# Optimization experiments

Measured on AMD Instinct MI355X. Metric: run time of the kernel, lower is better.

## Reference

```python
import jax, jax.numpy as jnp
from jax import lax
import numpy as np

C = 64          # channels
E = 8           # num_experts
K = 2           # active_experts
P = 8           # patch_size
EPS = 1e-5


def setup_inputs() -> dict:
    key = jax.random.key(0)
    ks = jax.random.split(key, 12)
    s = 0.05
    inp = {
        "x": jax.random.normal(ks[0], (2, C, 8, 128, 128), dtype=jnp.float32),
        # router Linear(C, E)
        "router_w": jax.random.normal(ks[1], (E, C), dtype=jnp.float32) * s,
        "router_b": jnp.zeros((E,), dtype=jnp.float32),
        # per-expert GatedConvBlock params, stacked over E
        "dw_w": jax.random.normal(ks[2], (E, C, 1, 1, 7, 7), dtype=jnp.float32) * s,   # depthwise (1,7,7)
        "dw_b": jnp.zeros((E, C), dtype=jnp.float32),
        "ln_w": jnp.ones((E, P, P), dtype=jnp.float32),
        "ln_b": jnp.zeros((E, P, P), dtype=jnp.float32),
        "pw_in_w": jax.random.normal(ks[3], (E, 2 * C, C), dtype=jnp.float32) * s,
        "pw_in_b": jnp.zeros((E, 2 * C), dtype=jnp.float32),
        "pw_out_w": jax.random.normal(ks[4], (E, C, C), dtype=jnp.float32) * s,
        "pw_out_b": jnp.zeros((E, C), dtype=jnp.float32),
    }
    return inp


def _gated_conv_block(x, dw_w, dw_b, ln_w, ln_b, pw_in_w, pw_in_b, pw_out_w, pw_out_b):
    # x: [N, C, L, P, P]
    res = x
    h = lax.conv_general_dilated(
        x, dw_w, window_strides=(1, 1, 1), padding="SAME",
        feature_group_count=x.shape[1],
        dimension_numbers=("NCDHW", "OIDHW", "NCDHW"),
    ) + dw_b[None, :, None, None, None]
    # LayerNorm over last two (spatial) dims with affine of shape [P, P]
    mu = jnp.mean(h, axis=(-2, -1), keepdims=True)
    var = jnp.var(h, axis=(-2, -1), keepdims=True)
    h = (h - mu) * lax.rsqrt(var + EPS) * ln_w + ln_b
    # pointwise conv in (1x1x1): C -> 2C
    h2 = jnp.einsum("oc,ncdhw->nodhw", pw_in_w, h) + pw_in_b[None, :, None, None, None]
    a, g = jnp.split(h2, 2, axis=1)
    h = jax.nn.silu(a) * g
    # pointwise conv out: C -> C
    h = jnp.einsum("oc,ncdhw->nodhw", pw_out_w, h) + pw_out_b[None, :, None, None, None]
    return res + h


def reference(x, router_w, router_b, dw_w, dw_b, ln_w, ln_b,
              pw_in_w, pw_in_b, pw_out_w, pw_out_b):
    B, Cc, L, H, W = x.shape
    nH, nW = H // P, W // P  # H, W chosen divisible by P (no padding path)
    N = B * nH * nW
    # patchify: [B,C,L,H,W] -> [N, C, L, P, P]
    xp = x.reshape(B, Cc, L, nH, P, nW, P).transpose(0, 3, 5, 1, 2, 4, 6)
    xp = xp.reshape(N, Cc, L, P, P)
    # router: mean over (L, P, P)
    router_in = jnp.mean(xp, axis=(2, 3, 4))                      # [N, C]
    logits = router_in @ router_w.T + router_b                    # [N, E]
    topv, topi = lax.top_k(logits, K)                             # [N, K]
    topw = jax.nn.softmax(topv, axis=1)                           # [N, K]
    # scatter top-k weights to dense [N, E] (zeros for unselected experts)
    wfull = jnp.zeros((N, E), dtype=x.dtype)
    wfull = wfull.at[jnp.arange(N)[:, None], topi].add(topw)
    out = jnp.zeros_like(xp)
    for e in range(E):  # fixed small expert count; each expert has distinct params
        ye = _gated_conv_block(xp, dw_w[e], dw_b[e], ln_w[e], ln_b[e],
                               pw_in_w[e], pw_in_b[e], pw_out_w[e], pw_out_b[e])
        out = out + wfull[:, e][:, None, None, None, None] * ye
    # unpatchify
    out = out.reshape(B, nH, nW, Cc, L, P, P).transpose(0, 3, 4, 1, 5, 2, 6)
    return out.reshape(B, Cc, L, H, W)
```

## Files before the change

kernel.cpp:

```cpp
#include <hip/hip_runtime.h>
#include <hip/hip_bf16.h>
#include <cstddef>
#include <cstdint>


typedef __attribute__((ext_vector_type(8))) short short8;
typedef __attribute__((ext_vector_type(4))) float f32x4;
typedef __attribute__((ext_vector_type(2))) float f32x2;

#define REPACK_NEED 68412416ull

__device__ __forceinline__ unsigned short f2bf(float f) {
  return __builtin_bit_cast(unsigned short, __float2bfloat16(f));
}
__device__ __forceinline__ float bflo(unsigned u) {
  return __builtin_bit_cast(float, u << 16);
}
__device__ __forceinline__ float bfhi(unsigned u) {
  return __builtin_bit_cast(float, u & 0xFFFF0000u);
}

__device__ __forceinline__ float wave_sum64(float v) {
#pragma unroll
  for (int m = 32; m > 0; m >>= 1) v += __shfl_xor(v, m, 64);
  return v;
}

__global__ void k_pre(const float* __restrict__ dw,
                      const float* __restrict__ pwin,
                      const float* __restrict__ pwout,
                      unsigned short* __restrict__ dwTbf,
                      unsigned short* __restrict__ wIn,
                      unsigned short* __restrict__ wOut) {
  int idx = blockIdx.x * 256 + threadIdx.x;
  if (idx < 25088) {
    int e = idx / 3136;
    int r = idx - e * 3136;
    int c = r / 49;
    int tap = r - c * 49;
    dwTbf[(e * 49 + tap) * 64 + c] = f2bf(dw[idx]);
  } else if (idx < 25088 + 65536) {
    int i = idx - 25088;
    wIn[i] = f2bf(pwin[i]);
  } else if (idx < 25088 + 65536 + 32768) {
    int i = idx - 90624;
    wOut[i] = f2bf(pwout[i]);
  }
}

__global__ __launch_bounds__(256) void k_sum(const float* __restrict__ x,
                                             float* __restrict__ partial_l) {
  __shared__ float red[256 * 17];
  int t = threadIdx.x, bid = blockIdx.x;
  int b = bid >> 8, c = (bid >> 2) & 63, lp = bid & 3;
  const float4* x4 = (const float4*)x + ((size_t)((b * 64 + c) * 8) + lp * 2) * 4096;
#pragma unroll 1
  for (int l2 = 0; l2 < 2; ++l2) {
    float acc[16];
#pragma unroll
    for (int k = 0; k < 16; ++k) acc[k] = 0.f;
#pragma unroll
    for (int k = 0; k < 16; ++k) {
      float4 v = x4[l2 * 4096 + k * 256 + t];
      acc[k] += v.x + v.y + v.z + v.w;
    }
    int pcol = (t & 31) >> 1;
    int slot = ((t & 1) << 3) | (t >> 5);
    __syncthreads();
#pragma unroll
    for (int k = 0; k < 16; ++k) red[(k * 16 + pcol) * 17 + slot] = acc[k];
    __syncthreads();
    float s = 0.f;
#pragma unroll
    for (int j = 0; j < 16; ++j) s += red[t * 17 + j];
    partial_l[((size_t)(b * 256 + t)) * 512 + (lp * 2 + l2) * 64 + c] = s;
  }
}

__global__ __launch_bounds__(256) void k_repack(const float* __restrict__ x,
                                                float* __restrict__ xr,
                                                float* __restrict__ partial_l) {
  __shared__ __align__(16) float lt[8 * 1060];
  int t = threadIdx.x, bid = blockIdx.x;
  int ct = bid & 7, hh = (bid >> 3) & 15, l = (bid >> 7) & 7, b = bid >> 10;
  int c0 = ct * 8;
  const float4* x4 = (const float4*)x;
  float4* xr4 = (float4*)xr;
  int y = t >> 5, xq = t & 31;
#pragma unroll
  for (int i = 0; i < 8; ++i) {
    size_t src = ((size_t)((b * 64 + c0 + i) * 8 + l) << 12) +
                 (size_t)(hh * 8 + y) * 32 + xq;
    float4 v = x4[src];
    *(float4*)(lt + i * 1060 + y * 132 + xq * 4) = v;
  }
  __syncthreads();
  int cc = (t >> 4) & 7, ihalf = t >> 7, pxq = t & 15;
  int py = pxq >> 1, xcol = pxq & 1;
#pragma unroll
  for (int iw = 0; iw < 8; ++iw) {
    int ww = ihalf * 8 + iw;
    float4 v = *(const float4*)(lt + cc * 1060 + py * 132 + ww * 8 + xcol * 4);
    int n = b * 256 + hh * 16 + ww;
    xr4[((size_t)(n * 8 + l) << 10) + (c0 + cc) * 16 + pxq] = v;
    float s = v.x + v.y + v.z + v.w;
#pragma unroll
    for (int m = 1; m < 16; m <<= 1) s += __shfl_xor(s, m, 64);
    if (pxq == 0) partial_l[(size_t)(n * 8 + l) * 64 + c0 + cc] = s;
  }
}

__global__ void k_router(const float* __restrict__ partial_l,
                         const float* __restrict__ rw, const float* __restrict__ rb,
                         int* __restrict__ sel_i, float* __restrict__ sel_w) {
  int n = blockIdx.x;
  int lane = threadIdx.x;
  float s = 0.f;
#pragma unroll
  for (int l = 0; l < 8; ++l)
    s += partial_l[(size_t)n * 512 + l * 64 + lane];
  float rin = s * (1.f / 512.f);
  float lg[8];
#pragma unroll
  for (int e = 0; e < 8; ++e) {
    float v = rin * rw[e * 64 + lane];
    lg[e] = wave_sum64(v) + rb[e];
  }
  int e0 = 0; float v0 = lg[0];
#pragma unroll
  for (int e = 1; e < 8; ++e) if (lg[e] > v0) { v0 = lg[e]; e0 = e; }
  int e1 = -1; float v1 = -1e30f;
#pragma unroll
  for (int e = 0; e < 8; ++e) if (e != e0 && lg[e] > v1) { v1 = lg[e]; e1 = e; }
  if (lane == 0) {
    float w1 = __expf(v1 - v0);
    float z = 1.f + w1;
    sel_i[2 * n] = e0; sel_i[2 * n + 1] = e1;
    sel_w[2 * n] = 1.f / z; sel_w[2 * n + 1] = w1 / z;
  }
}

template <bool REPACK>
__global__ __launch_bounds__(512) void k_main(
    const float* __restrict__ x, const float* __restrict__ xr,
    const unsigned short* __restrict__ dwTbf, const float* __restrict__ dwb,
    const float* __restrict__ lnw, const float* __restrict__ lnb,
    const float* __restrict__ pwin_b, const float* __restrict__ pwout_b,
    const unsigned short* __restrict__ wInBf,
    const unsigned short* __restrict__ wOutBf,
    const int* __restrict__ sel_i, const float* __restrict__ sel_w,
    float* __restrict__ out) {
  __shared__ __align__(16) char smem[49408];
  unsigned* wsdw       = (unsigned*)smem;
  unsigned short* B1   = (unsigned short*)(smem + 12544);
  unsigned short* B2   = (unsigned short*)(smem + 21760);
  unsigned short* B3   = (unsigned short*)(smem + 30976);
  f32x2* ln2           = (f32x2*)(smem + 30976);
  unsigned short* xsb  = (unsigned short*)(smem + 40192);
  float* eb            = (float*)(smem + 21760);

  const int t = threadIdx.x;
  const int lane = t & 63;
  const int wv = __builtin_amdgcn_readfirstlane(t >> 6);
  const int wi = wv >> 1;
  const int jh = wv & 1;
  const int r15 = lane & 15, r4 = lane >> 4;
  const int bidx = blockIdx.x;
  const int n = bidx >> 3, l = bidx & 7;
  const int b = n >> 8, p = n & 255;
  const int hh = p >> 4, ww = p & 15;
  const size_t obase = (size_t)b * 8388608 + (size_t)l * 16384 +
                       (size_t)hh * 1024 + (size_t)ww * 8;

  const int e0 = __builtin_amdgcn_readfirstlane(sel_i[2 * n]);
  const int e1 = __builtin_amdgcn_readfirstlane(sel_i[2 * n + 1]);
  const float we0 = sel_w[2 * n];
  const float we1 = sel_w[2 * n + 1];

#pragma unroll
  for (int it = 0; it < 2; ++it) {
    int g = it * 512 + t;
    int c = g >> 4, q = g & 15;
    float4 v;
    if constexpr (REPACK)
      v = ((const float4*)xr)[(size_t)bidx * 1024 + g];
    else
      v = *(const float4*)(x + obase + (size_t)c * 131072 + (q >> 1) * 128 + (q & 1) * 4);
    int rs = (q >> 1) ^ ((c >> 3) & 7);
    uint2 w2;
    w2.x = (unsigned)f2bf(v.x) | ((unsigned)f2bf(v.y) << 16);
    w2.y = (unsigned)f2bf(v.z) | ((unsigned)f2bf(v.w) << 16);
    *(uint2*)(xsb + c * 72 + rs * 8 + (q & 1) * 4) = w2;
  }
  {
    const unsigned short* s0 = dwTbf + (size_t)e0 * 3136;
    const unsigned short* s1 = dwTbf + (size_t)e1 * 3136;
#pragma unroll
    for (int i = 0; i < 6; ++i) {
      int idx = i * 512 + t;
      wsdw[idx] = (unsigned)s0[idx] | ((unsigned)s1[idx] << 16);
    }
    if (t < 64) wsdw[3072 + t] = (unsigned)s0[3072 + t] | ((unsigned)s1[3072 + t] << 16);
  }
  __syncthreads();

  f32x2 hva[4], hvb[4];
  {
    const float bias0 = dwb[e0 * 64 + lane];
    const float bias1 = dwb[e1 * 64 + lane];
#pragma unroll
    for (int j = 0; j < 4; ++j) {
      hva[j] = f32x2{bias0, bias0};
      hvb[j] = f32x2{bias1, bias1};
    }
  }
  {
    const unsigned short* rowbase = xsb + lane * 72;
    const int rc = (lane >> 3) & 7;
    const unsigned* wl = wsdw + lane;
    const int y0 = wv;
    const int rlo = (y0 - 3 < 0) ? 0 : y0 - 3;
    const int rhi = (y0 + 3 > 7) ? 7 : y0 + 3;
    for (int r = rlo; r <= rhi; ++r) {
      uint4 xraw = *(const uint4*)(rowbase + (r ^ rc) * 8);
      float xp[14];
      xp[0] = 0.f; xp[1] = 0.f; xp[2] = 0.f;
      xp[3] = bflo(xraw.x); xp[4] = bfhi(xraw.x);
      xp[5] = bflo(xraw.y); xp[6] = bfhi(xraw.y);
      xp[7] = bflo(xraw.z); xp[8] = bfhi(xraw.z);
      xp[9] = bflo(xraw.w); xp[10] = bfhi(xraw.w);
      xp[11] = 0.f; xp[12] = 0.f; xp[13] = 0.f;
      f32x2 pr[13];
#pragma unroll
      for (int m = 0; m < 13; ++m) pr[m] = f32x2{xp[m], xp[m + 1]};
      const unsigned* wrow = wl + (r - y0 + 3) * 448;
#pragma unroll
      for (int dx = 0; dx < 7; ++dx) {
        unsigned wp = wrow[dx * 64];
        float wt0 = bflo(wp);
        float wt1 = bfhi(wp);
        f32x2 w20 = f32x2{wt0, wt0};
        f32x2 w21 = f32x2{wt1, wt1};
        hva[0] = __builtin_elementwise_fma(pr[dx + 0], w20, hva[0]);
        hva[1] = __builtin_elementwise_fma(pr[dx + 2], w20, hva[1]);
        hva[2] = __builtin_elementwise_fma(pr[dx + 4], w20, hva[2]);
        hva[3] = __builtin_elementwise_fma(pr[dx + 6], w20, hva[3]);
        hvb[0] = __builtin_elementwise_fma(pr[dx + 0], w21, hvb[0]);
        hvb[1] = __builtin_elementwise_fma(pr[dx + 2], w21, hvb[1]);
        hvb[2] = __builtin_elementwise_fma(pr[dx + 4], w21, hvb[2]);
        hvb[3] = __builtin_elementwise_fma(pr[dx + 6], w21, hvb[3]);
      }
    }
  }
  {
    f32x2 psa = f32x2{0.f, 0.f}, pqa = f32x2{0.f, 0.f};
    f32x2 psb = f32x2{0.f, 0.f}, pqb = f32x2{0.f, 0.f};
#pragma unroll
    for (int j = 0; j < 4; ++j) {
      psa += hva[j];
      pqa = __builtin_elementwise_fma(hva[j], hva[j], pqa);
      psb += hvb[j];
      pqb = __builtin_elementwise_fma(hvb[j], hvb[j], pqb);
    }
    ln2[(0 * 8 + wv) * 64 + lane] = f32x2{psa.x + psa.y, pqa.x + pqa.y};
    ln2[(1 * 8 + wv) * 64 + lane] = f32x2{psb.x + psb.y, pqb.x + pqb.y};
  }
  __syncthreads();

  {
    float sm0 = 0.f, sq0 = 0.f, sm1 = 0.f, sq1 = 0.f;
#pragma unroll
    for (int w = 0; w < 8; ++w) {
      f32x2 va = ln2[(0 * 8 + w) * 64 + lane];
      f32x2 vb = ln2[(1 * 8 + w) * 64 + lane];
      sm0 += va.x; sq0 += va.y;
      sm1 += vb.x; sq1 += vb.y;
    }
    float mu0 = sm0 * (1.f / 64.f);
    float rstd0 = rsqrtf(sq0 * (1.f / 64.f) - mu0 * mu0 + 1e-5f);
    float mu1 = sm1 * (1.f / 64.f);
    float rstd1 = rsqrtf(sq1 * (1.f / 64.f) - mu1 * mu1 + 1e-5f);
#pragma unroll
    for (int j = 0; j < 8; ++j) {
      int s = wv * 8 + j;
      float ha = (j & 1) ? hva[j >> 1].y : hva[j >> 1].x;
      float hb = (j & 1) ? hvb[j >> 1].y : hvb[j >> 1].x;
      float nv0 = (ha - mu0) * rstd0 * lnw[e0 * 64 + s] + lnb[e0 * 64 + s];
      float nv1 = (hb - mu1) * rstd1 * lnw[e1 * 64 + s] + lnb[e1 * 64 + s];
      B1[s * 72 + lane] = f2bf(nv0);
      B2[s * 72 + lane] = f2bf(nv1);
    }
  }
  __syncthreads();

  float oacc[8];
#pragma unroll
  for (int i = 0; i < 8; ++i) oacc[i] = 0.f;

  {
    const unsigned short* wInE = wInBf + (size_t)e0 * 8192;
    short8 aA[2], aG[2];
#pragma unroll
    for (int kf = 0; kf < 2; ++kf) {
      aA[kf] = *(const short8*)(wInE + (16 * wi + r15) * 64 + kf * 32 + r4 * 8);
      aG[kf] = *(const short8*)(wInE + (64 + 16 * wi + r15) * 64 + kf * 32 + r4 * 8);
    }
    f32x4 accA[2], accG[2];
#pragma unroll
    for (int ntl = 0; ntl < 2; ++ntl)
#pragma unroll
      for (int v = 0; v < 4; ++v) {
        accA[ntl][v] = pwin_b[e0 * 128 + 16 * wi + r4 * 4 + v];
        accG[ntl][v] = pwin_b[e0 * 128 + 64 + 16 * wi + r4 * 4 + v];
      }
#pragma unroll
    for (int ntl = 0; ntl < 2; ++ntl) {
      const int nt = 2 * jh + ntl;
#pragma unroll
      for (int kf = 0; kf < 2; ++kf) {
        short8 bfr = *(const short8*)(B1 + (16 * nt + r15) * 72 + kf * 32 + r4 * 8);
        accA[ntl] = __builtin_amdgcn_mfma_f32_16x16x32_bf16(aA[kf], bfr, accA[ntl], 0, 0, 0);
        accG[ntl] = __builtin_amdgcn_mfma_f32_16x16x32_bf16(aG[kf], bfr, accG[ntl], 0, 0, 0);
      }
    }
#pragma unroll
    for (int ntl = 0; ntl < 2; ++ntl) {
      const int nt = 2 * jh + ntl;
      float hval[4];
#pragma unroll
      for (int v = 0; v < 4; ++v) {
        float a = accA[ntl][v];
        float g = accG[ntl][v];
        hval[v] = __fdividef(a, 1.f + __expf(-a)) * g;
      }
      uint2 w2;
      w2.x = (unsigned)f2bf(hval[0]) | ((unsigned)f2bf(hval[1]) << 16);
      w2.y = (unsigned)f2bf(hval[2]) | ((unsigned)f2bf(hval[3]) << 16);
      *(uint2*)(B3 + (16 * nt + r15) * 72 + 16 * wi + 4 * r4) = w2;
    }
  }
  __syncthreads();

  {
    const unsigned short* wOutE = wOutBf + (size_t)e0 * 4096;
    short8 aO[2];
#pragma unroll
    for (int kf = 0; kf < 2; ++kf)
      aO[kf] = *(const short8*)(wOutE + (16 * wi + r15) * 64 + kf * 32 + r4 * 8);
    f32x4 accO[2];
#pragma unroll
    for (int ntl = 0; ntl < 2; ++ntl)
#pragma unroll
      for (int v = 0; v < 4; ++v) accO[ntl][v] = 0.f;
#pragma unroll
    for (int ntl = 0; ntl < 2; ++ntl) {
      const int nt = 2 * jh + ntl;
#pragma unroll
      for (int kf = 0; kf < 2; ++kf) {
        short8 bfr = *(const short8*)(B3 + (16 * nt + r15) * 72 + kf * 32 + r4 * 8);
        accO[ntl] = __builtin_amdgcn_mfma_f32_16x16x32_bf16(aO[kf], bfr, accO[ntl], 0, 0, 0);
      }
    }
    float bO[4];
#pragma unroll
    for (int v = 0; v < 4; ++v) bO[v] = pwout_b[e0 * 64 + 16 * wi + r4 * 4 + v];
#pragma unroll
    for (int ntl = 0; ntl < 2; ++ntl)
#pragma unroll
      for (int v = 0; v < 4; ++v) oacc[ntl * 4 + v] += we0 * (accO[ntl][v] + bO[v]);

    const unsigned short* wInE = wInBf + (size_t)e1 * 8192;
    short8 aA[2], aG[2];
#pragma unroll
    for (int kf = 0; kf < 2; ++kf) {
      aA[kf] = *(const short8*)(wInE + (16 * wi + r15) * 64 + kf * 32 + r4 * 8);
      aG[kf] = *(const short8*)(wInE + (64 + 16 * wi + r15) * 64 + kf * 32 + r4 * 8);
    }
    f32x4 accA[2], accG[2];
#pragma unroll
    for (int ntl = 0; ntl < 2; ++ntl)
#pragma unroll
      for (int v = 0; v < 4; ++v) {
        accA[ntl][v] = pwin_b[e1 * 128 + 16 * wi + r4 * 4 + v];
        accG[ntl][v] = pwin_b[e1 * 128 + 64 + 16 * wi + r4 * 4 + v];
      }
#pragma unroll
    for (int ntl = 0; ntl < 2; ++ntl) {
      const int nt = 2 * jh + ntl;
#pragma unroll
      for (int kf = 0; kf < 2; ++kf) {
        short8 bfr = *(const short8*)(B2 + (16 * nt + r15) * 72 + kf * 32 + r4 * 8);
        accA[ntl] = __builtin_amdgcn_mfma_f32_16x16x32_bf16(aA[kf], bfr, accA[ntl], 0, 0, 0);
        accG[ntl] = __builtin_amdgcn_mfma_f32_16x16x32_bf16(aG[kf], bfr, accG[ntl], 0, 0, 0);
      }
    }
#pragma unroll
    for (int ntl = 0; ntl < 2; ++ntl) {
      const int nt = 2 * jh + ntl;
      float hval[4];
#pragma unroll
      for (int v = 0; v < 4; ++v) {
        float a = accA[ntl][v];
        float g = accG[ntl][v];
        hval[v] = __fdividef(a, 1.f + __expf(-a)) * g;
      }
      uint2 w2;
      w2.x = (unsigned)f2bf(hval[0]) | ((unsigned)f2bf(hval[1]) << 16);
      w2.y = (unsigned)f2bf(hval[2]) | ((unsigned)f2bf(hval[3]) << 16);
      *(uint2*)(B1 + (16 * nt + r15) * 72 + 16 * wi + 4 * r4) = w2;
    }
  }
  __syncthreads();

  {
    const unsigned short* wOutE = wOutBf + (size_t)e1 * 4096;
    short8 aO[2];
#pragma unroll
    for (int kf = 0; kf < 2; ++kf)
      aO[kf] = *(const short8*)(wOutE + (16 * wi + r15) * 64 + kf * 32 + r4 * 8);
    f32x4 accO[2];
#pragma unroll
    for (int ntl = 0; ntl < 2; ++ntl)
#pragma unroll
      for (int v = 0; v < 4; ++v) accO[ntl][v] = 0.f;
#pragma unroll
    for (int ntl = 0; ntl < 2; ++ntl) {
      const int nt = 2 * jh + ntl;
#pragma unroll
      for (int kf = 0; kf < 2; ++kf) {
        short8 bfr = *(const short8*)(B1 + (16 * nt + r15) * 72 + kf * 32 + r4 * 8);
        accO[ntl] = __builtin_amdgcn_mfma_f32_16x16x32_bf16(aO[kf], bfr, accO[ntl], 0, 0, 0);
      }
    }
    float bO[4];
#pragma unroll
    for (int v = 0; v < 4; ++v) bO[v] = pwout_b[e1 * 64 + 16 * wi + r4 * 4 + v];
#pragma unroll
    for (int ntl = 0; ntl < 2; ++ntl)
#pragma unroll
      for (int v = 0; v < 4; ++v) oacc[ntl * 4 + v] += we1 * (accO[ntl][v] + bO[v]);
  }
#pragma unroll
  for (int ntl = 0; ntl < 2; ++ntl)
#pragma unroll
    for (int v = 0; v < 4; ++v)
      eb[(16 * wi + 4 * r4 + v) * 68 + 16 * (2 * jh + ntl) + r15] = oacc[ntl * 4 + v];
  __syncthreads();

#pragma unroll
  for (int it = 0; it < 2; ++it) {
    int g = it * 512 + t;
    int c = g >> 4, q = g & 15;
    float4 dv = *(const float4*)(eb + c * 68 + q * 4);
    float4 xv;
    if constexpr (REPACK)
      xv = ((const float4*)xr)[(size_t)bidx * 1024 + g];
    else
      xv = *(const float4*)(x + obase + (size_t)c * 131072 + (q >> 1) * 128 + (q & 1) * 4);
    float4 o4 = {xv.x + dv.x, xv.y + dv.y, xv.z + dv.z, xv.w + dv.w};
    *(float4*)(out + obase + (size_t)c * 131072 + (q >> 1) * 128 + (q & 1) * 4) = o4;
  }
}

extern "C" void kernel_launch(void* const* d_in, const int* in_sizes, int n_in,
                              void* d_out, int out_size, void* d_ws, size_t ws_size,
                              hipStream_t stream) {
  const float* x       = (const float*)d_in[0];
  const float* rw      = (const float*)d_in[1];
  const float* rb      = (const float*)d_in[2];
  const float* dww     = (const float*)d_in[3];
  const float* dwb     = (const float*)d_in[4];
  const float* lnw     = (const float*)d_in[5];
  const float* lnb     = (const float*)d_in[6];
  const float* pwin_w  = (const float*)d_in[7];
  const float* pwin_b  = (const float*)d_in[8];
  const float* pwout_w = (const float*)d_in[9];
  const float* pwout_b = (const float*)d_in[10];
  float* out = (float*)d_out;

  char* ws = (char*)d_ws;
  float*          partial_l = (float*)ws;
  unsigned short* dwTbf     = (unsigned short*)(ws + 1048576);
  int*            sel_i     = (int*)(ws + 1098752);
  float*          sel_w     = (float*)(ws + 1102848);
  unsigned short* wInBf     = (unsigned short*)(ws + 1106944);
  unsigned short* wOutBf    = (unsigned short*)(ws + 1238016);
  float*          xr        = (float*)(ws + 1303552);

  const bool repack = ws_size >= REPACK_NEED;

  hipLaunchKernelGGL(k_pre, dim3(482), dim3(256), 0, stream,
                     dww, pwin_w, pwout_w, dwTbf, wInBf, wOutBf);
  if (repack)
    hipLaunchKernelGGL(k_repack, dim3(2048), dim3(256), 0, stream, x, xr, partial_l);
  else
    hipLaunchKernelGGL(k_sum, dim3(512), dim3(256), 0, stream, x, partial_l);
  hipLaunchKernelGGL(k_router, dim3(512), dim3(64), 0, stream,
                     partial_l, rw, rb, sel_i, sel_w);
  if (repack)
    hipLaunchKernelGGL((k_main<true>), dim3(4096), dim3(512), 0, stream,
                       x, xr, dwTbf, dwb, lnw, lnb, pwin_b, pwout_b,
                       wInBf, wOutBf, sel_i, sel_w, out);
  else
    hipLaunchKernelGGL((k_main<false>), dim3(4096), dim3(512), 0, stream,
                       x, xr, dwTbf, dwb, lnw, lnb, pwin_b, pwout_b,
                       wInBf, wOutBf, sel_i, sel_w, out);
}
```

Before: 114.2 us.

## Fuse weight preconversion into repack kernel and shrink main kernel LDS footprint

The bf16 weight conversion is folded into the repack kernel as extra blocks, which removes one kernel launch on the repack path. In the main kernel, the second expert's layernorm output is written only after the first expert's output projection finishes. This lets the buffers be reused and cuts shared memory from about 49KB to about 40KB per block, aiming for higher occupancy. The cost is an extra barrier and more serialization between the two expert passes.

```diff
diff --git a/kernel.cpp b/kernel.cpp
--- a/kernel.cpp
+++ b/kernel.cpp
@@ -26,13 +26,13 @@
   return v;
 }
 
-__global__ void k_pre(const float* __restrict__ dw,
-                      const float* __restrict__ pwin,
-                      const float* __restrict__ pwout,
-                      unsigned short* __restrict__ dwTbf,
-                      unsigned short* __restrict__ wIn,
-                      unsigned short* __restrict__ wOut) {
-  int idx = blockIdx.x * 256 + threadIdx.x;
+__device__ __forceinline__ void pre_body(int idx,
+                                         const float* __restrict__ dw,
+                                         const float* __restrict__ pwin,
+                                         const float* __restrict__ pwout,
+                                         unsigned short* __restrict__ dwTbf,
+                                         unsigned short* __restrict__ wIn,
+                                         unsigned short* __restrict__ wOut) {
   if (idx < 25088) {
     int e = idx / 3136;
     int r = idx - e * 3136;
@@ -48,6 +48,15 @@
   }
 }
 
+__global__ void k_pre(const float* __restrict__ dw,
+                      const float* __restrict__ pwin,
+                      const float* __restrict__ pwout,
+                      unsigned short* __restrict__ dwTbf,
+                      unsigned short* __restrict__ wIn,
+                      unsigned short* __restrict__ wOut) {
+  pre_body(blockIdx.x * 256 + threadIdx.x, dw, pwin, pwout, dwTbf, wIn, wOut);
+}
+
 __global__ __launch_bounds__(256) void k_sum(const float* __restrict__ x,
                                              float* __restrict__ partial_l) {
   __shared__ float red[256 * 17];
@@ -77,11 +86,18 @@
   }
 }
 
-__global__ __launch_bounds__(256) void k_repack(const float* __restrict__ x,
-                                                float* __restrict__ xr,
-                                                float* __restrict__ partial_l) {
+__global__ __launch_bounds__(256) void k_repack(
+    const float* __restrict__ x, float* __restrict__ xr,
+    float* __restrict__ partial_l,
+    const float* __restrict__ dw, const float* __restrict__ pwin,
+    const float* __restrict__ pwout, unsigned short* __restrict__ dwTbf,
+    unsigned short* __restrict__ wIn, unsigned short* __restrict__ wOut) {
+  int t = threadIdx.x, bid = blockIdx.x;
+  if (bid >= 2048) {
+    pre_body((bid - 2048) * 256 + t, dw, pwin, pwout, dwTbf, wIn, wOut);
+    return;
+  }
   __shared__ __align__(16) float lt[8 * 1060];
-  int t = threadIdx.x, bid = blockIdx.x;
   int ct = bid & 7, hh = (bid >> 3) & 15, l = (bid >> 7) & 7, b = bid >> 10;
   int c0 = ct * 8;
   const float4* x4 = (const float4*)x;
@@ -150,14 +166,13 @@
     const unsigned short* __restrict__ wOutBf,
     const int* __restrict__ sel_i, const float* __restrict__ sel_w,
     float* __restrict__ out) {
-  __shared__ __align__(16) char smem[49408];
+  __shared__ __align__(16) char smem[40192];
   unsigned* wsdw       = (unsigned*)smem;
   unsigned short* B1   = (unsigned short*)(smem + 12544);
   unsigned short* B2   = (unsigned short*)(smem + 21760);
-  unsigned short* B3   = (unsigned short*)(smem + 30976);
-  f32x2* ln2           = (f32x2*)(smem + 30976);
-  unsigned short* xsb  = (unsigned short*)(smem + 40192);
-  float* eb            = (float*)(smem + 21760);
+  f32x2* ln2           = (f32x2*)(smem + 21760);
+  unsigned short* xsb  = (unsigned short*)(smem + 30976);
+  float* eb            = (float*)smem;
 
   const int t = threadIdx.x;
   const int lane = t & 63;
@@ -267,6 +282,7 @@
   }
   __syncthreads();
 
+  float mu1, rstd1;
   {
     float sm0 = 0.f, sq0 = 0.f, sm1 = 0.f, sq1 = 0.f;
 #pragma unroll
@@ -278,17 +294,14 @@
     }
     float mu0 = sm0 * (1.f / 64.f);
     float rstd0 = rsqrtf(sq0 * (1.f / 64.f) - mu0 * mu0 + 1e-5f);
-    float mu1 = sm1 * (1.f / 64.f);
-    float rstd1 = rsqrtf(sq1 * (1.f / 64.f) - mu1 * mu1 + 1e-5f);
+    mu1 = sm1 * (1.f / 64.f);
+    rstd1 = rsqrtf(sq1 * (1.f / 64.f) - mu1 * mu1 + 1e-5f);
 #pragma unroll
     for (int j = 0; j < 8; ++j) {
       int s = wv * 8 + j;
       float ha = (j & 1) ? hva[j >> 1].y : hva[j >> 1].x;
-      float hb = (j & 1) ? hvb[j >> 1].y : hvb[j >> 1].x;
       float nv0 = (ha - mu0) * rstd0 * lnw[e0 * 64 + s] + lnb[e0 * 64 + s];
-      float nv1 = (hb - mu1) * rstd1 * lnw[e1 * 64 + s] + lnb[e1 * 64 + s];
       B1[s * 72 + lane] = f2bf(nv0);
-      B2[s * 72 + lane] = f2bf(nv1);
     }
   }
   __syncthreads();
@@ -336,12 +349,19 @@
       uint2 w2;
       w2.x = (unsigned)f2bf(hval[0]) | ((unsigned)f2bf(hval[1]) << 16);
       w2.y = (unsigned)f2bf(hval[2]) | ((unsigned)f2bf(hval[3]) << 16);
-      *(uint2*)(B3 + (16 * nt + r15) * 72 + 16 * wi + 4 * r4) = w2;
-    }
-  }
-  __syncthreads();
-
-  {
+      *(uint2*)(B2 + (16 * nt + r15) * 72 + 16 * wi + 4 * r4) = w2;
+    }
+  }
+  __syncthreads();
+
+  {
+#pragma unroll
+    for (int j = 0; j < 8; ++j) {
+      int s = wv * 8 + j;
+      float hb = (j & 1) ? hvb[j >> 1].y : hvb[j >> 1].x;
+      float nv1 = (hb - mu1) * rstd1 * lnw[e1 * 64 + s] + lnb[e1 * 64 + s];
+      B1[s * 72 + lane] = f2bf(nv1);
+    }
     const unsigned short* wOutE = wOutBf + (size_t)e0 * 4096;
     short8 aO[2];
 #pragma unroll
@@ -357,7 +377,7 @@
       const int nt = 2 * jh + ntl;
 #pragma unroll
       for (int kf = 0; kf < 2; ++kf) {
-        short8 bfr = *(const short8*)(B3 + (16 * nt + r15) * 72 + kf * 32 + r4 * 8);
+        short8 bfr = *(const short8*)(B2 + (16 * nt + r15) * 72 + kf * 32 + r4 * 8);
         accO[ntl] = __builtin_amdgcn_mfma_f32_16x16x32_bf16(aO[kf], bfr, accO[ntl], 0, 0, 0);
       }
     }
@@ -368,7 +388,10 @@
     for (int ntl = 0; ntl < 2; ++ntl)
 #pragma unroll
       for (int v = 0; v < 4; ++v) oacc[ntl * 4 + v] += we0 * (accO[ntl][v] + bO[v]);
-
+  }
+  __syncthreads();
+
+  {
     const unsigned short* wInE = wInBf + (size_t)e1 * 8192;
     short8 aA[2], aG[2];
 #pragma unroll
@@ -389,7 +412,7 @@
       const int nt = 2 * jh + ntl;
 #pragma unroll
       for (int kf = 0; kf < 2; ++kf) {
-        short8 bfr = *(const short8*)(B2 + (16 * nt + r15) * 72 + kf * 32 + r4 * 8);
+        short8 bfr = *(const short8*)(B1 + (16 * nt + r15) * 72 + kf * 32 + r4 * 8);
         accA[ntl] = __builtin_amdgcn_mfma_f32_16x16x32_bf16(aA[kf], bfr, accA[ntl], 0, 0, 0);
         accG[ntl] = __builtin_amdgcn_mfma_f32_16x16x32_bf16(aG[kf], bfr, accG[ntl], 0, 0, 0);
       }
@@ -407,7 +430,7 @@
       uint2 w2;
       w2.x = (unsigned)f2bf(hval[0]) | ((unsigned)f2bf(hval[1]) << 16);
       w2.y = (unsigned)f2bf(hval[2]) | ((unsigned)f2bf(hval[3]) << 16);
-      *(uint2*)(B1 + (16 * nt + r15) * 72 + 16 * wi + 4 * r4) = w2;
+      *(uint2*)(B2 + (16 * nt + r15) * 72 + 16 * wi + 4 * r4) = w2;
     }
   }
   __syncthreads();
@@ -428,7 +451,7 @@
       const int nt = 2 * jh + ntl;
 #pragma unroll
       for (int kf = 0; kf < 2; ++kf) {
-        short8 bfr = *(const short8*)(B1 + (16 * nt + r15) * 72 + kf * 32 + r4 * 8);
+        short8 bfr = *(const short8*)(B2 + (16 * nt + r15) * 72 + kf * 32 + r4 * 8);
         accO[ntl] = __builtin_amdgcn_mfma_f32_16x16x32_bf16(aO[kf], bfr, accO[ntl], 0, 0, 0);
       }
     }
@@ -489,12 +512,14 @@
 
   const bool repack = ws_size >= REPACK_NEED;
 
-  hipLaunchKernelGGL(k_pre, dim3(482), dim3(256), 0, stream,
-                     dww, pwin_w, pwout_w, dwTbf, wInBf, wOutBf);
-  if (repack)
-    hipLaunchKernelGGL(k_repack, dim3(2048), dim3(256), 0, stream, x, xr, partial_l);
-  else
+  if (repack) {
+    hipLaunchKernelGGL(k_repack, dim3(2544), dim3(256), 0, stream,
+                       x, xr, partial_l, dww, pwin_w, pwout_w, dwTbf, wInBf, wOutBf);
+  } else {
+    hipLaunchKernelGGL(k_pre, dim3(496), dim3(256), 0, stream,
+                       dww, pwin_w, pwout_w, dwTbf, wInBf, wOutBf);
     hipLaunchKernelGGL(k_sum, dim3(512), dim3(256), 0, stream, x, partial_l);
+  }
   hipLaunchKernelGGL(k_router, dim3(512), dim3(64), 0, stream,
                      partial_l, rw, rb, sel_i, sel_w);
   if (repack)
```

Result: slower. 122.6 us (+7.3%).
